# Performance work log

Measured on AMD Instinct MI355X. Metric: run time of the kernel, lower is better.

## Reference

```python
import jax, jax.numpy as jnp
import numpy as np

B, N, C = 16, 4096, 91            # images, proposals/image, classes (incl. background)
H, W = 800.0, 1333.0              # image shape
SCORE_THRESH = 0.05
NMS_THRESH = 0.5
K = 100                           # detections_per_img (greedy NMS steps)
M = 4096                          # top-M candidate prefilter before NMS
OFFSET = 1.0e4                    # class offset for batched NMS (>> max coord)
DW_CLAMP = float(np.log(1000.0 / 16.0))


def setup_inputs():
    key = jax.random.key(0)
    k1, k2, k3, k4, k5, k6 = jax.random.split(key, 6)
    class_logits = jax.random.normal(k1, (B * N, C), jnp.float32) * 2.0
    box_regression = jax.random.normal(k2, (B * N, C * 4), jnp.float32) * 0.1
    # valid proposal boxes (x1 < x2, y1 < y2, inside image)
    x1 = jax.random.uniform(k3, (B, N, 1)) * (W - 64.0)
    y1 = jax.random.uniform(k4, (B, N, 1)) * (H - 64.0)
    bw = jax.random.uniform(k5, (B, N, 1)) * 256.0 + 16.0
    bh = jax.random.uniform(k6, (B, N, 1)) * 256.0 + 16.0
    proposals = jnp.concatenate([x1, y1, jnp.minimum(x1 + bw, W), jnp.minimum(y1 + bh, H)], -1)
    return {"class_logits": class_logits, "box_regression": box_regression, "proposals": proposals}


def _decode_and_clip(rel, props):
    w = props[..., 2] - props[..., 0]
    h = props[..., 3] - props[..., 1]
    cx = props[..., 0] + 0.5 * w
    cy = props[..., 1] + 0.5 * h
    dx = rel[..., 0] / 10.0
    dy = rel[..., 1] / 10.0
    dw = jnp.minimum(rel[..., 2] / 5.0, DW_CLAMP)
    dh = jnp.minimum(rel[..., 3] / 5.0, DW_CLAMP)
    pcx = dx * w[..., None] + cx[..., None]
    pcy = dy * h[..., None] + cy[..., None]
    pw = jnp.exp(dw) * w[..., None]
    ph = jnp.exp(dh) * h[..., None]
    boxes = jnp.stack([
        jnp.clip(pcx - 0.5 * pw, 0.0, W),
        jnp.clip(pcy - 0.5 * ph, 0.0, H),
        jnp.clip(pcx + 0.5 * pw, 0.0, W),
        jnp.clip(pcy + 0.5 * ph, 0.0, H)], -1)  # [B,N,C,4]
    return boxes


def _greedy_nms(boxes, scores):
    # boxes: [M,4] (already class-offset), scores: [M] (suppressed entries == -1)
    x1, y1, x2, y2 = boxes[:, 0], boxes[:, 1], boxes[:, 2], boxes[:, 3]
    area = (x2 - x1) * (y2 - y1)

    def step(sc, _):
        i = jnp.argmax(sc)
        s = sc[i]
        valid = s > 0.0
        iw = jnp.clip(jnp.minimum(x2, x2[i]) - jnp.maximum(x1, x1[i]), 0.0)
        ih = jnp.clip(jnp.minimum(y2, y2[i]) - jnp.maximum(y1, y1[i]), 0.0)
        inter = iw * ih
        iou = inter / (area + area[i] - inter + 1e-9)
        sc = jnp.where((iou > NMS_THRESH) & valid, -1.0, sc)
        sc = sc.at[i].set(-1.0)
        return sc, (i, s, valid)

    _, (idx, ss, vv) = jax.lax.scan(step, scores, None, length=K)
    return idx, ss, vv


def _post_image(boxes_all, scores_all):
    # boxes_all: [N,C,4] decoded+clipped, scores_all: [N,C] softmax scores
    boxes = boxes_all[:, 1:, :].reshape(-1, 4)          # drop background class 0
    scores = scores_all[:, 1:].reshape(-1)              # [N*(C-1)], class fastest
    labels = jnp.tile(jnp.arange(1, C, dtype=jnp.int32), N)
    scores = jnp.where(scores > SCORE_THRESH, scores, -1.0)
    top_s, top_i = jax.lax.top_k(scores, M)
    b = boxes[top_i]
    l = labels[top_i]
    ob = b + (l.astype(jnp.float32) * OFFSET)[:, None]  # batched_nms class-offset trick
    idx, ss, vv = _greedy_nms(ob, top_s)
    out_boxes = jnp.where(vv[:, None], b[idx], 0.0)     # [K,4]
    out_scores = jnp.where(vv, ss, 0.0)                 # [K]
    out_labels = jnp.where(vv, l[idx], -1)              # [K]
    return out_boxes, out_scores, out_labels, vv


def reference(class_logits, box_regression, proposals):
    pred_scores = jax.nn.softmax(class_logits, -1).reshape(B, N, C)
    rel = box_regression.reshape(B, N, C, 4)
    pred_boxes = _decode_and_clip(rel, proposals)
    boxes, scores, labels, valid = jax.vmap(_post_image)(pred_boxes, pred_scores)
    return boxes, scores, labels, valid
```

## Files before the change

### kernel.cpp

```cpp
#include <hip/hip_runtime.h>

typedef unsigned long long u64;
typedef unsigned int u32;

#define BDIM 16
#define NP   4096
#define NC   91
#define NCM1 90
#define MSEL 4096
#define NSORT 1024
#define KOUT 100
#define RSLOT 19
#define CAP_D (NP * RSLOT)
#define SCORE_T 0.05f
#define NMS_T   0.5f
#define OFFSETF 10000.0f
#define DW_CLAMP_F 4.135166556742356f
#define WF 1333.0f
#define HF 800.0f
#define GTMIN 384
#define HCAP 4096
#define FKEY (((u64)0x3E800000u) << 32)

#define TN 1024
#define RPB 64

#define DECODE_BODY(kvar, bvar, BOXDST, PACKDST)                                   \
    {                                                                              \
        int flat = (int)(~(u32)(kvar));                                            \
        int nidx = flat / NCM1;                                                    \
        int c    = flat - nidx * NCM1 + 1;                                         \
        const float* pr = props + ((long)(bvar) * NP + nidx) * 4;                  \
        float x1 = pr[0], y1 = pr[1], x2 = pr[2], y2 = pr[3];                      \
        float w = x2 - x1, h = y2 - y1;                                            \
        float cx = x1 + 0.5f * w, cy = y1 + 0.5f * h;                              \
        const float* rr = boxreg + (((long)(bvar) * NP + nidx) * NC + c) * 4;      \
        float dx = rr[0] / 10.0f, dy = rr[1] / 10.0f;                              \
        float dw = fminf(rr[2] / 5.0f, DW_CLAMP_F);                                \
        float dh = fminf(rr[3] / 5.0f, DW_CLAMP_F);                                \
        float pcx = __fadd_rn(__fmul_rn(dx, w), cx);                               \
        float pcy = __fadd_rn(__fmul_rn(dy, h), cy);                               \
        float pw  = __fmul_rn(expf(dw), w);                                        \
        float ph2 = __fmul_rn(expf(dh), h);                                        \
        float bx1 = fminf(fmaxf(pcx - 0.5f * pw, 0.0f), WF);                       \
        float by1 = fminf(fmaxf(pcy - 0.5f * ph2, 0.0f), HF);                      \
        float bx2 = fminf(fmaxf(pcx + 0.5f * pw, 0.0f), WF);                       \
        float by2 = fminf(fmaxf(pcy + 0.5f * ph2, 0.0f), HF);                      \
        BOXDST = make_float4(bx1, by1, bx2, by2);                                  \
        float offB = (float)c * OFFSETF;                                           \
        float ox1 = bx1 + offB, oy1 = by1 + offB;                                  \
        float ox2 = bx2 + offB, oy2 = by2 + offB;                                  \
        PACKDST = make_float2((ox2 - ox1) * (oy2 - oy1), (float)c);                \
    }

__global__ __launch_bounds__(1024) void k_zero(int* __restrict__ gcount,
                                               int* __restrict__ hcnt,
                                               int* __restrict__ ghist) {
    int blk = blockIdx.x;
    if (blk == 0) {
        if (threadIdx.x < BDIM) gcount[threadIdx.x] = 0;
        if (threadIdx.x >= 64 && threadIdx.x < 64 + BDIM) hcnt[threadIdx.x - 64] = 0;
    } else {
        int* g = ghist + (blk - 1) * 2048;
        for (int i = threadIdx.x; i < 2048; i += 1024) g[i] = 0;
    }
}

__global__ __launch_bounds__(256) void k_soft(const float* __restrict__ logits,
                                              u64* __restrict__ dense,
                                              int* __restrict__ gcount,
                                              u64* __restrict__ hot,
                                              int* __restrict__ hcnt,
                                              int* __restrict__ ghist) {
    __shared__ u64 stage[RPB * RSLOT];
    __shared__ u64 hstage[256];
    __shared__ int lhist[2048];
    __shared__ int s_cnt, s_base, s_hcnt, s_hbase;

    int blk  = blockIdx.x;
    int b    = blk >> 6;
    int lane = threadIdx.x & 63;
    int wid  = threadIdx.x >> 6;

    if (threadIdx.x == 0) { s_cnt = 0; s_hcnt = 0; }
    for (int i = threadIdx.x; i < 2048; i += 256) lhist[i] = 0;
    __syncthreads();

    u64 lm = (1ull << lane) - 1ull;
    for (int it = 0; it < RPB / 4; ++it) {
        int row = blk * RPB + it * 4 + wid;
        const float* lg = logits + (long)row * NC;

        float v0 = lg[lane];
        float v1 = (lane < NC - 64) ? lg[64 + lane] : -3.0e38f;
        float mx = fmaxf(v0, v1);
#pragma unroll
        for (int s = 32; s; s >>= 1) mx = fmaxf(mx, __shfl_xor(mx, s));
        float e0 = expf(v0 - mx);
        float e1 = (lane < NC - 64) ? expf(v1 - mx) : 0.0f;
        float sum = e0 + e1;
#pragma unroll
        for (int s = 32; s; s >>= 1) sum += __shfl_xor(sum, s);

        float s0 = e0 / sum;
        float s1 = e1 / sum;

        int n = row & (NP - 1);
        bool p0 = (lane >= 1) && (s0 > SCORE_T);
        bool p1 = (lane < NC - 64) && (s1 > SCORE_T);
        u64 key0 = ((u64)__float_as_uint(s0) << 32) | (u32)(~(u32)(n * NCM1 + (lane - 1)));
        u64 key1 = ((u64)__float_as_uint(s1) << 32) | (u32)(~(u32)(n * NCM1 + (64 + lane - 1)));
        u64 m0 = __ballot(p0);
        u64 m1 = __ballot(p1);
        int c0  = __popcll(m0);
        int cnt = c0 + __popcll(m1);

        int base = 0;
        if (lane == 0 && cnt) base = atomicAdd(&s_cnt, cnt);
        base = __shfl(base, 0);
        if (p0) {
            stage[base + __popcll(m0 & lm)] = key0;
            atomicAdd(&lhist[(int)(key0 >> 53)], 1);
        }
        if (p1) {
            stage[base + c0 + __popcll(m1 & lm)] = key1;
            atomicAdd(&lhist[(int)(key1 >> 53)], 1);
        }

        bool q0 = p0 && (s0 >= 0.25f);
        bool q1 = p1 && (s1 >= 0.25f);
        u64 h0 = __ballot(q0);
        u64 h1 = __ballot(q1);
        int hc0 = __popcll(h0);
        int hrow = hc0 + __popcll(h1);
        int hb = 0;
        if (lane == 0 && hrow) hb = atomicAdd(&s_hcnt, hrow);
        hb = __shfl(hb, 0);
        if (q0) hstage[hb + __popcll(h0 & lm)] = key0;
        if (q1) hstage[hb + hc0 + __popcll(h1 & lm)] = key1;
    }
    __syncthreads();

    if (threadIdx.x == 0) {
        s_base  = atomicAdd(&gcount[b], s_cnt);
        s_hbase = atomicAdd(&hcnt[b], s_hcnt);
    }
    __syncthreads();
    int m = s_cnt, base = s_base;
    u64* kb = dense + (long)b * CAP_D + base;
    for (int i = threadIdx.x; i < m; i += 256) kb[i] = stage[i];
    int hm = s_hcnt, hb2 = s_hbase;
    u64* hbp = hot + (long)b * HCAP;
    for (int i = threadIdx.x; i < hm; i += 256) {
        int pos = hb2 + i;
        if (pos < HCAP) hbp[pos] = hstage[i];
    }
    for (int i = threadIdx.x; i < 2048; i += 256) {
        int v = lhist[i];
        if (v) atomicAdd(&ghist[b * 2048 + i], v);
    }
}

__device__ __forceinline__ u64 radix_rank(const u64* __restrict__ kb, int n, int rank,
                                          int* hist, int* p_sel, int* p_gt, int tid) {
    u64 prefix = 0, mask = 0;
    const int shifts[6] = {53, 42, 31, 20, 10, 0};
    const int bitsv [6] = {11, 11, 11, 11, 10, 10};

    for (int pass = 0; pass < 6; ++pass) {
        int shift = shifts[pass];
        int nb = 1 << bitsv[pass];
        if (tid < nb) hist[tid] = 0;
        if (tid + 1024 < nb) hist[tid + 1024] = 0;
        __syncthreads();
        for (int i = tid; i < n; i += 1024) {
            u64 k = kb[i];
            if ((k & mask) == prefix)
                atomicAdd(&hist[(int)((k >> shift) & (u64)(nb - 1))], 1);
        }
        __syncthreads();
        for (int d = 1; d < nb; d <<= 1) {
            int v0 = 0, v1 = 0;
            if (tid < nb && tid + d < nb) v0 = hist[tid + d];
            if (tid + 1024 < nb && tid + 1024 + d < nb) v1 = hist[tid + 1024 + d];
            __syncthreads();
            if (tid < nb) hist[tid] += v0;
            if (tid + 1024 < nb) hist[tid + 1024] += v1;
            __syncthreads();
        }
        for (int j = tid; j < nb; j += 1024) {
            int c  = hist[j];
            int cn = (j + 1 < nb) ? hist[j + 1] : 0;
            if (c >= rank && cn < rank) { *p_sel = j; *p_gt = cn; }
        }
        __syncthreads();
        prefix |= ((u64)(*p_sel)) << shift;
        mask   |= ((u64)(nb - 1)) << shift;
        rank   -= *p_gt;
        __syncthreads();
    }
    return prefix;
}

__device__ __forceinline__ u64 radix_upper(const u64* __restrict__ kb, int n, int rank,
                                           int* hist, int* p_sel, int* p_gt, int tid) {
    int rank0 = rank;
    u64 prefix = 0, mask = 0;
    const int shifts[6] = {53, 42, 31, 20, 10, 0};
    const int bitsv [6] = {11, 11, 11, 11, 10, 10};

    for (int pass = 0; pass < 6; ++pass) {
        int shift = shifts[pass];
        int nb = 1 << bitsv[pass];
        if (tid < nb) hist[tid] = 0;
        if (tid + 1024 < nb) hist[tid + 1024] = 0;
        __syncthreads();
        for (int i = tid; i < n; i += 1024) {
            u64 k = kb[i];
            if ((k & mask) == prefix)
                atomicAdd(&hist[(int)((k >> shift) & (u64)(nb - 1))], 1);
        }
        __syncthreads();
        for (int d = 1; d < nb; d <<= 1) {
            int v0 = 0, v1 = 0;
            if (tid < nb && tid + d < nb) v0 = hist[tid + d];
            if (tid + 1024 < nb && tid + 1024 + d < nb) v1 = hist[tid + 1024 + d];
            __syncthreads();
            if (tid < nb) hist[tid] += v0;
            if (tid + 1024 < nb) hist[tid + 1024] += v1;
            __syncthreads();
        }
        for (int j = tid; j < nb; j += 1024) {
            int c  = hist[j];
            int cn = (j + 1 < nb) ? hist[j + 1] : 0;
            if (c >= rank && cn < rank) { *p_sel = j; *p_gt = cn; }
        }
        __syncthreads();
        int sel = *p_sel, gt = *p_gt;
        rank -= gt;
        __syncthreads();
        if (pass < 5) {
            if (rank0 - rank >= GTMIN)
                return prefix + ((u64)(sel + 1) << shift);
            prefix |= ((u64)sel) << shift;
            mask   |= ((u64)(nb - 1)) << shift;
        } else {
            prefix |= ((u64)sel) << shift;
        }
    }
    return prefix;
}

__global__ __launch_bounds__(TN) void k_post(const u64* __restrict__ dense,
                                             const int* __restrict__ gcount,
                                             const u64* __restrict__ hot,
                                             const int* __restrict__ hcnt,
                                             const int* __restrict__ ghist,
                                             const float* __restrict__ boxreg,
                                             const float* __restrict__ props,
                                             float* __restrict__ out) {
    __shared__ __align__(16) char ldsbuf[131072];
    __shared__ int s_cnt, s_nacc, s_sel, s_gt;

    float4* sbox  = (float4*)ldsbuf;
    float2* spack = (float2*)(ldsbuf + 16384);
    u64*    skey  = (u64*)(ldsbuf + 24576);
    int*    hist  = (int*)(ldsbuf + 32768);

    int b = blockIdx.x, tid = threadIdx.x;
    int lane = tid & 63, wid = tid >> 6;
    int n = gcount[b]; if (n > CAP_D) n = CAP_D;
    const u64* kb = dense + (long)b * CAP_D;
    u64 lm = (1ull << lane) - 1ull;
    int npad = (n + TN - 1) & ~(TN - 1);

    u64 Bthr = 0ull;
    bool hist_ok = false;
    if (n > NSORT) {
        for (int i = tid; i < 2048; i += TN) hist[i] = ghist[b * 2048 + i];
        __syncthreads();
        for (int d = 1; d < 2048; d <<= 1) {
            int v0 = 0, v1 = 0;
            if (tid + d < 2048) v0 = hist[tid + d];
            if (tid + 1024 + d < 2048) v1 = hist[tid + 1024 + d];
            __syncthreads();
            hist[tid] += v0;
            if (tid + 1024 + d < 2048 || tid + 1024 < 2048) hist[tid + 1024] += v1;
            __syncthreads();
        }
        for (int j = tid; j < 2048; j += TN) {
            int c  = hist[j];
            int cn = (j + 1 < 2048) ? hist[j + 1] : 0;
            if (c >= NSORT && cn < NSORT) { s_sel = j; s_gt = cn; }
        }
        __syncthreads();
        int sel = s_sel, gt = s_gt;
        __syncthreads();
        if (gt >= GTMIN) { Bthr = ((u64)(sel + 1)) << 53; hist_ok = true; }
        else             Bthr = radix_upper(kb, n, NSORT, hist, &s_sel, &s_gt, tid);
    }
    int hn = hcnt[b];
    bool use_hot = hist_ok && (Bthr >= FKEY) && (hn <= HCAP);

    skey[tid] = 0ull;
    if (tid == 0) s_cnt = 0;
    __syncthreads();
    if (use_hot) {
        const u64* hb = hot + (long)b * HCAP;
        int hpad = (hn + TN - 1) & ~(TN - 1);
        for (int i0 = tid; i0 < hpad; i0 += TN) {
            bool inb = (i0 < hn);
            u64 k = inb ? hb[i0] : 0ull;
            bool pred = inb && (k >= Bthr);
            u64 mb_ = __ballot(pred);
            int cnt = __popcll(mb_);
            int bp = 0;
            if (lane == 0 && cnt) bp = atomicAdd(&s_cnt, cnt);
            bp = __shfl(bp, 0);
            if (pred) {
                int pos = bp + __popcll(mb_ & lm);
                if (pos < NSORT) skey[pos] = k;
            }
        }
    } else {
        for (int i0 = tid; i0 < npad; i0 += TN) {
            bool inb = (i0 < n);
            u64 k = inb ? kb[i0] : 0ull;
            bool pred = inb && (k >= Bthr);
            u64 mb_ = __ballot(pred);
            int cnt = __popcll(mb_);
            int bp = 0;
            if (lane == 0 && cnt) bp = atomicAdd(&s_cnt, cnt);
            bp = __shfl(bp, 0);
            if (pred) {
                int pos = bp + __popcll(mb_ & lm);
                if (pos < NSORT) skey[pos] = k;
            }
        }
    }
    __syncthreads();
    if (s_cnt > NSORT) {
        Bthr = radix_upper(kb, n, NSORT, hist, &s_sel, &s_gt, tid);
        skey[tid] = 0ull;
        if (tid == 0) s_cnt = 0;
        __syncthreads();
        for (int i0 = tid; i0 < npad; i0 += TN) {
            bool inb = (i0 < n);
            u64 k = inb ? kb[i0] : 0ull;
            bool pred = inb && (k >= Bthr);
            u64 mb_ = __ballot(pred);
            int cnt = __popcll(mb_);
            int bp = 0;
            if (lane == 0 && cnt) bp = atomicAdd(&s_cnt, cnt);
            bp = __shfl(bp, 0);
            if (pred) {
                int pos = bp + __popcll(mb_ & lm);
                if (pos < NSORT) skey[pos] = k;
            }
        }
        __syncthreads();
    }
    int mb = s_cnt; if (mb > NSORT) mb = NSORT;

    {
        u64 r = skey[tid];
        for (int kk = 2; kk <= NSORT; kk <<= 1) {
            for (int j = kk >> 1; j; j >>= 1) {
                u64 p;
                if (j >= 64) {
                    skey[tid] = r;
                    __syncthreads();
                    p = skey[tid ^ j];
                    __syncthreads();
                } else {
                    p = __shfl_xor(r, j);
                }
                bool lower = (tid & j) == 0;
                bool desc  = ((tid & kk) == 0);
                u64 mx = (r > p) ? r : p;
                u64 mn = (r > p) ? p : r;
                r = (lower == desc) ? mx : mn;
            }
        }
        skey[tid] = r;
        __syncthreads();
    }

    for (int i = tid; i < mb; i += TN) {
        u64 k = skey[i];
        float4 bx; float2 pk;
        DECODE_BODY(k, b, bx, pk);
        sbox[i] = bx;
        spack[i] = pk;
    }
    __syncthreads();

    float ax1_0 = 0, ay1_0 = 0, ax2_0 = 0, ay2_0 = 0, aar_0 = 0;
    float ax1_1 = 0, ay1_1 = 0, ax2_1 = 0, ay2_1 = 0, aar_1 = 0;
    int alb_0 = -1, alb_1 = -1;
    u64 aky_0 = 0, aky_1 = 0;
    int nacc = 0;

    if (wid == 0) {
        float4 Bv = sbox[0];
        float2 pk = spack[0];
        u64    ck = skey[0];
        for (int i = 0; i < mb && nacc < KOUT; ++i) {
            int ip = (i + 1 < mb) ? i + 1 : i;
            float4 nBv = sbox[ip];
            float2 npk = spack[ip];
            u64    nck = skey[ip];

            float areaB = pk.x;
            float labf  = pk.y;
            float off   = __fmul_rn(labf, OFFSETF);
            bool conf = false;
            if (lane < nacc && (float)alb_0 == labf) {
                float op1x = __fadd_rn(fminf(ax2_0, Bv.z), off);
                float op2x = __fadd_rn(fmaxf(ax1_0, Bv.x), off);
                float iw = fmaxf(op1x - op2x, 0.0f);
                float op1y = __fadd_rn(fminf(ay2_0, Bv.w), off);
                float op2y = __fadd_rn(fmaxf(ay1_0, Bv.y), off);
                float ih = fmaxf(op1y - op2y, 0.0f);
                float inter = iw * ih;
                float denom = areaB + aar_0 - inter + 1e-9f;
                if (inter / denom > NMS_T) conf = true;
            }
            if (64 + lane < nacc && (float)alb_1 == labf) {
                float op1x = __fadd_rn(fminf(ax2_1, Bv.z), off);
                float op2x = __fadd_rn(fmaxf(ax1_1, Bv.x), off);
                float iw = fmaxf(op1x - op2x, 0.0f);
                float op1y = __fadd_rn(fminf(ay2_1, Bv.w), off);
                float op2y = __fadd_rn(fmaxf(ay1_1, Bv.y), off);
                float ih = fmaxf(op1y - op2y, 0.0f);
                float inter = iw * ih;
                float denom = areaB + aar_1 - inter + 1e-9f;
                if (inter / denom > NMS_T) conf = true;
            }
            if (__ballot(conf) == 0ull) {
                if (nacc < 64) {
                    if (lane == nacc) {
                        ax1_0 = Bv.x; ay1_0 = Bv.y; ax2_0 = Bv.z; ay2_0 = Bv.w;
                        aar_0 = areaB; alb_0 = (int)labf; aky_0 = ck;
                    }
                } else {
                    if (lane == nacc - 64) {
                        ax1_1 = Bv.x; ay1_1 = Bv.y; ax2_1 = Bv.z; ay2_1 = Bv.w;
                        aar_1 = areaB; alb_1 = (int)labf; aky_1 = ck;
                    }
                }
                ++nacc;
            }
            Bv = nBv; pk = npk; ck = nck;
        }
        if (lane == 0) s_nacc = nacc;
    }
    __syncthreads();

    if (s_nacc < KOUT && Bthr != 0ull) {
        u64 T = 0ull;
        if (n > MSEL) T = radix_rank(kb, n, MSEL, hist, &s_sel, &s_gt, tid);

        u64*    fkey  = (u64*)ldsbuf;
        float4* fbox  = (float4*)(ldsbuf + 32768);
        float2* fpack = (float2*)(ldsbuf + 98304);

        for (int i = tid; i < MSEL; i += TN) fkey[i] = 0ull;
        if (tid == 0) s_cnt = 0;
        __syncthreads();
        for (int i0 = tid; i0 < npad; i0 += TN) {
            bool inb = (i0 < n);
            u64 k = inb ? kb[i0] : 0ull;
            bool pred = inb && (k >= T && k < Bthr);
            u64 mb_ = __ballot(pred);
            int cnt = __popcll(mb_);
            int bp = 0;
            if (lane == 0 && cnt) bp = atomicAdd(&s_cnt, cnt);
            bp = __shfl(bp, 0);
            if (pred) {
                int pos = bp + __popcll(mb_ & lm);
                if (pos < MSEL) fkey[pos] = k;
            }
        }
        __syncthreads();
        int mb2 = s_cnt; if (mb2 > MSEL) mb2 = MSEL;

        for (int kk = 2; kk <= MSEL; kk <<= 1) {
            for (int j = kk >> 1; j > 0; j >>= 1) {
                for (int t = tid; t < MSEL; t += TN) {
                    int l = t ^ j;
                    if (l > t) {
                        u64 a = fkey[t], c = fkey[l];
                        bool up = ((t & kk) == 0);
                        bool sw = up ? (a < c) : (a > c);
                        if (sw) { fkey[t] = c; fkey[l] = a; }
                    }
                }
                __syncthreads();
            }
        }

        for (int i = tid; i < mb2; i += TN) {
            u64 k = fkey[i];
            float4 bx; float2 pk;
            DECODE_BODY(k, b, bx, pk);
            fbox[i] = bx;
            fpack[i] = pk;
        }
        __syncthreads();

        if (wid == 0) {
            float4 Bv = fbox[0];
            float2 pk = fpack[0];
            u64    ck = fkey[0];
            for (int i = 0; i < mb2 && nacc < KOUT; ++i) {
                int ip = (i + 1 < mb2) ? i + 1 : i;
                float4 nBv = fbox[ip];
                float2 npk = fpack[ip];
                u64    nck = fkey[ip];

                float areaB = pk.x;
                float labf  = pk.y;
                float off   = __fmul_rn(labf, OFFSETF);
                bool conf = false;
                if (lane < nacc && (float)alb_0 == labf) {
                    float op1x = __fadd_rn(fminf(ax2_0, Bv.z), off);
                    float op2x = __fadd_rn(fmaxf(ax1_0, Bv.x), off);
                    float iw = fmaxf(op1x - op2x, 0.0f);
                    float op1y = __fadd_rn(fminf(ay2_0, Bv.w), off);
                    float op2y = __fadd_rn(fmaxf(ay1_0, Bv.y), off);
                    float ih = fmaxf(op1y - op2y, 0.0f);
                    float inter = iw * ih;
                    float denom = areaB + aar_0 - inter + 1e-9f;
                    if (inter / denom > NMS_T) conf = true;
                }
                if (64 + lane < nacc && (float)alb_1 == labf) {
                    float op1x = __fadd_rn(fminf(ax2_1, Bv.z), off);
                    float op2x = __fadd_rn(fmaxf(ax1_1, Bv.x), off);
                    float iw = fmaxf(op1x - op2x, 0.0f);
                    float op1y = __fadd_rn(fminf(ay2_1, Bv.w), off);
                    float op2y = __fadd_rn(fmaxf(ay1_1, Bv.y), off);
                    float ih = fmaxf(op1y - op2y, 0.0f);
                    float inter = iw * ih;
                    float denom = areaB + aar_1 - inter + 1e-9f;
                    if (inter / denom > NMS_T) conf = true;
                }
                if (__ballot(conf) == 0ull) {
                    if (nacc < 64) {
                        if (lane == nacc) {
                            ax1_0 = Bv.x; ay1_0 = Bv.y; ax2_0 = Bv.z; ay2_0 = Bv.w;
                            aar_0 = areaB; alb_0 = (int)labf; aky_0 = ck;
                        }
                    } else {
                        if (lane == nacc - 64) {
                            ax1_1 = Bv.x; ay1_1 = Bv.y; ax2_1 = Bv.z; ay2_1 = Bv.w;
                            aar_1 = areaB; alb_1 = (int)labf; aky_1 = ck;
                        }
                    }
                    ++nacc;
                }
                Bv = nBv; pk = npk; ck = nck;
            }
            if (lane == 0) s_nacc = nacc;
        }
        __syncthreads();
    }

    int na = s_nacc; if (na > KOUT) na = KOUT;
    if (wid == 0) {
        if (lane < na) {
            int a = lane;
            float* ob = out + ((long)b * KOUT + a) * 4;
            ob[0] = ax1_0; ob[1] = ay1_0; ob[2] = ax2_0; ob[3] = ay2_0;
            out[BDIM * KOUT * 4 + b * KOUT + a] = __uint_as_float((u32)(aky_0 >> 32));
            out[BDIM * KOUT * 5 + b * KOUT + a] = (float)alb_0;
            out[BDIM * KOUT * 6 + b * KOUT + a] = 1.0f;
        }
        if (64 + lane < na) {
            int a = 64 + lane;
            float* ob = out + ((long)b * KOUT + a) * 4;
            ob[0] = ax1_1; ob[1] = ay1_1; ob[2] = ax2_1; ob[3] = ay2_1;
            out[BDIM * KOUT * 4 + b * KOUT + a] = __uint_as_float((u32)(aky_1 >> 32));
            out[BDIM * KOUT * 5 + b * KOUT + a] = (float)alb_1;
            out[BDIM * KOUT * 6 + b * KOUT + a] = 1.0f;
        }
    }
    for (int a = tid; a < KOUT; a += TN) {
        if (a >= na) {
            float* ob = out + ((long)b * KOUT + a) * 4;
            ob[0] = 0.0f; ob[1] = 0.0f; ob[2] = 0.0f; ob[3] = 0.0f;
            out[BDIM * KOUT * 4 + b * KOUT + a] = 0.0f;
            out[BDIM * KOUT * 5 + b * KOUT + a] = -1.0f;
            out[BDIM * KOUT * 6 + b * KOUT + a] = 0.0f;
        }
    }
}

extern "C" void kernel_launch(void* const* d_in, const int* in_sizes, int n_in,
                              void* d_out, int out_size, void* d_ws, size_t ws_size,
                              hipStream_t stream) {
    const float* logits = (const float*)d_in[0];
    const float* boxreg = (const float*)d_in[1];
    const float* props  = (const float*)d_in[2];
    float* out = (float*)d_out;

    char* ws = (char*)d_ws;
    int* gcount = (int*)(ws + 0);
    int* hcnt   = (int*)(ws + 256);
    int* ghist  = (int*)(ws + 1024);
    u64* hot    = (u64*)(ws + 132096);
    u64* dense  = (u64*)(ws + 1048576);

    k_zero<<<17, 1024, 0, stream>>>(gcount, hcnt, ghist);
    k_soft<<<(BDIM * NP) / RPB, 256, 0, stream>>>(logits, dense, gcount, hot, hcnt, ghist);
    k_post<<<BDIM, TN, 0, stream>>>(dense, gcount, hot, hcnt, ghist, boxreg, props, out);
}
```

Measured before the change: 78.55 us.

## Precompute parallel IoU suppression bitmasks for first 128 candidates before greedy NMS

Each thread computes a 128-bit suppression mask against the first 128 sorted candidates in parallel. A single wavefront then runs greedy NMS with bitmask ANDs instead of per-step IoU and ballot. If all KOUT detections come from the first 128 candidates, the accepted boxes are gathered directly. Otherwise it falls back to the original serial loop. This adds an O(128·mb) parallel IoU pass and extra LDS use to shorten the serial dependency chain.

```diff
diff --git a/kernel.cpp b/kernel.cpp
--- a/kernel.cpp
+++ b/kernel.cpp
@@ -260,12 +260,15 @@
                                              const float* __restrict__ props,
                                              float* __restrict__ out) {
     __shared__ __align__(16) char ldsbuf[131072];
-    __shared__ int s_cnt, s_nacc, s_sel, s_gt;
+    __shared__ int s_cnt, s_nacc, s_sel, s_gt, s_ok;
+    __shared__ int s_ord[KOUT];
 
     float4* sbox  = (float4*)ldsbuf;
     float2* spack = (float2*)(ldsbuf + 16384);
     u64*    skey  = (u64*)(ldsbuf + 24576);
     int*    hist  = (int*)(ldsbuf + 32768);
+    u64*    mlo   = (u64*)(ldsbuf + 40960);
+    u64*    mhi   = (u64*)(ldsbuf + 49152);
 
     int b = blockIdx.x, tid = threadIdx.x;
     int lane = tid & 63, wid = tid >> 6;
@@ -395,129 +398,88 @@
     }
     __syncthreads();
 
+    {
+        int i = tid;
+        if (i < mb) {
+            float4 Bv = sbox[i];
+            float2 pk = spack[i];
+            float areaB = pk.x, labf = pk.y;
+            float off = __fmul_rn(labf, OFFSETF);
+            u64 lo = 0, hi = 0;
+            int jmax = (mb < 128) ? mb : 128;
+            for (int j = 0; j < jmax; ++j) {
+                if (j != i) {
+                    float2 tp = spack[j];
+                    if (tp.y == labf) {
+                        float4 Tv = sbox[j];
+                        float op1x = __fadd_rn(fminf(Tv.z, Bv.z), off);
+                        float op2x = __fadd_rn(fmaxf(Tv.x, Bv.x), off);
+                        float iw = fmaxf(op1x - op2x, 0.0f);
+                        float op1y = __fadd_rn(fminf(Tv.w, Bv.w), off);
+                        float op2y = __fadd_rn(fmaxf(Tv.y, Bv.y), off);
+                        float ih = fmaxf(op1y - op2y, 0.0f);
+                        float inter = iw * ih;
+                        float denom = areaB + tp.x - inter + 1e-9f;
+                        float iou = inter / denom;
+                        if (iou > NMS_T) { if (j < 64) lo |= 1ull << j; else hi |= 1ull << (j - 64); }
+                    }
+                }
+            }
+            mlo[i] = lo; mhi[i] = hi;
+        }
+    }
+    __syncthreads();
+
+    if (wid == 0) {
+        int fn = 0; int ok = 1;
+        u64 alo = 0, ahi = 0;
+        for (int i = 0; i < mb && fn < KOUT; ++i) {
+            u64 lo = mlo[i], hi = mhi[i];
+            if (((lo & alo) | (hi & ahi)) == 0ull) {
+                if (lane == 0) s_ord[fn] = i;
+                ++fn;
+                if (i < 64) alo |= 1ull << i;
+                else if (i < 128) ahi |= 1ull << (i - 64);
+                else if (fn < KOUT) { ok = 0; break; }
+            }
+        }
+        if (lane == 0) { s_nacc = fn; s_ok = ok; }
+    }
+    __syncthreads();
+
     float ax1_0 = 0, ay1_0 = 0, ax2_0 = 0, ay2_0 = 0, aar_0 = 0;
     float ax1_1 = 0, ay1_1 = 0, ax2_1 = 0, ay2_1 = 0, aar_1 = 0;
     int alb_0 = -1, alb_1 = -1;
     u64 aky_0 = 0, aky_1 = 0;
     int nacc = 0;
 
-    if (wid == 0) {
-        float4 Bv = sbox[0];
-        float2 pk = spack[0];
-        u64    ck = skey[0];
-        for (int i = 0; i < mb && nacc < KOUT; ++i) {
-            int ip = (i + 1 < mb) ? i + 1 : i;
-            float4 nBv = sbox[ip];
-            float2 npk = spack[ip];
-            u64    nck = skey[ip];
-
-            float areaB = pk.x;
-            float labf  = pk.y;
-            float off   = __fmul_rn(labf, OFFSETF);
-            bool conf = false;
-            if (lane < nacc && (float)alb_0 == labf) {
-                float op1x = __fadd_rn(fminf(ax2_0, Bv.z), off);
-                float op2x = __fadd_rn(fmaxf(ax1_0, Bv.x), off);
-                float iw = fmaxf(op1x - op2x, 0.0f);
-                float op1y = __fadd_rn(fminf(ay2_0, Bv.w), off);
-                float op2y = __fadd_rn(fmaxf(ay1_0, Bv.y), off);
-                float ih = fmaxf(op1y - op2y, 0.0f);
-                float inter = iw * ih;
-                float denom = areaB + aar_0 - inter + 1e-9f;
-                if (inter / denom > NMS_T) conf = true;
-            }
-            if (64 + lane < nacc && (float)alb_1 == labf) {
-                float op1x = __fadd_rn(fminf(ax2_1, Bv.z), off);
-                float op2x = __fadd_rn(fmaxf(ax1_1, Bv.x), off);
-                float iw = fmaxf(op1x - op2x, 0.0f);
-                float op1y = __fadd_rn(fminf(ay2_1, Bv.w), off);
-                float op2y = __fadd_rn(fmaxf(ay1_1, Bv.y), off);
-                float ih = fmaxf(op1y - op2y, 0.0f);
-                float inter = iw * ih;
-                float denom = areaB + aar_1 - inter + 1e-9f;
-                if (inter / denom > NMS_T) conf = true;
-            }
-            if (__ballot(conf) == 0ull) {
-                if (nacc < 64) {
-                    if (lane == nacc) {
-                        ax1_0 = Bv.x; ay1_0 = Bv.y; ax2_0 = Bv.z; ay2_0 = Bv.w;
-                        aar_0 = areaB; alb_0 = (int)labf; aky_0 = ck;
-                    }
-                } else {
-                    if (lane == nacc - 64) {
-                        ax1_1 = Bv.x; ay1_1 = Bv.y; ax2_1 = Bv.z; ay2_1 = Bv.w;
-                        aar_1 = areaB; alb_1 = (int)labf; aky_1 = ck;
-                    }
-                }
-                ++nacc;
-            }
-            Bv = nBv; pk = npk; ck = nck;
-        }
-        if (lane == 0) s_nacc = nacc;
-    }
-    __syncthreads();
-
-    if (s_nacc < KOUT && Bthr != 0ull) {
-        u64 T = 0ull;
-        if (n > MSEL) T = radix_rank(kb, n, MSEL, hist, &s_sel, &s_gt, tid);
-
-        u64*    fkey  = (u64*)ldsbuf;
-        float4* fbox  = (float4*)(ldsbuf + 32768);
-        float2* fpack = (float2*)(ldsbuf + 98304);
-
-        for (int i = tid; i < MSEL; i += TN) fkey[i] = 0ull;
-        if (tid == 0) s_cnt = 0;
-        __syncthreads();
-        for (int i0 = tid; i0 < npad; i0 += TN) {
-            bool inb = (i0 < n);
-            u64 k = inb ? kb[i0] : 0ull;
-            bool pred = inb && (k >= T && k < Bthr);
-            u64 mb_ = __ballot(pred);
-            int cnt = __popcll(mb_);
-            int bp = 0;
-            if (lane == 0 && cnt) bp = atomicAdd(&s_cnt, cnt);
-            bp = __shfl(bp, 0);
-            if (pred) {
-                int pos = bp + __popcll(mb_ & lm);
-                if (pos < MSEL) fkey[pos] = k;
-            }
-        }
-        __syncthreads();
-        int mb2 = s_cnt; if (mb2 > MSEL) mb2 = MSEL;
-
-        for (int kk = 2; kk <= MSEL; kk <<= 1) {
-            for (int j = kk >> 1; j > 0; j >>= 1) {
-                for (int t = tid; t < MSEL; t += TN) {
-                    int l = t ^ j;
-                    if (l > t) {
-                        u64 a = fkey[t], c = fkey[l];
-                        bool up = ((t & kk) == 0);
-                        bool sw = up ? (a < c) : (a > c);
-                        if (sw) { fkey[t] = c; fkey[l] = a; }
-                    }
-                }
-                __syncthreads();
-            }
-        }
-
-        for (int i = tid; i < mb2; i += TN) {
-            u64 k = fkey[i];
-            float4 bx; float2 pk;
-            DECODE_BODY(k, b, bx, pk);
-            fbox[i] = bx;
-            fpack[i] = pk;
-        }
-        __syncthreads();
-
+    if (s_ok) {
         if (wid == 0) {
-            float4 Bv = fbox[0];
-            float2 pk = fpack[0];
-            u64    ck = fkey[0];
-            for (int i = 0; i < mb2 && nacc < KOUT; ++i) {
-                int ip = (i + 1 < mb2) ? i + 1 : i;
-                float4 nBv = fbox[ip];
-                float2 npk = fpack[ip];
-                u64    nck = fkey[ip];
+            int fn = s_nacc;
+            if (lane < fn) {
+                int i = s_ord[lane];
+                float4 Bv = sbox[i]; float2 pk = spack[i];
+                ax1_0 = Bv.x; ay1_0 = Bv.y; ax2_0 = Bv.z; ay2_0 = Bv.w;
+                aar_0 = pk.x; alb_0 = (int)pk.y; aky_0 = skey[i];
+            }
+            if (64 + lane < fn) {
+                int i = s_ord[64 + lane];
+                float4 Bv = sbox[i]; float2 pk = spack[i];
+                ax1_1 = Bv.x; ay1_1 = Bv.y; ax2_1 = Bv.z; ay2_1 = Bv.w;
+                aar_1 = pk.x; alb_1 = (int)pk.y; aky_1 = skey[i];
+            }
+            nacc = fn;
+        }
+    } else {
+        if (wid == 0) {
+            float4 Bv = sbox[0];
+            float2 pk = spack[0];
+            u64    ck = skey[0];
+            for (int i = 0; i < mb && nacc < KOUT; ++i) {
+                int ip = (i + 1 < mb) ? i + 1 : i;
+                float4 nBv = sbox[ip];
+                float2 npk = spack[ip];
+                u64    nck = skey[ip];
 
                 float areaB = pk.x;
                 float labf  = pk.y;
@@ -563,6 +525,116 @@
             }
             if (lane == 0) s_nacc = nacc;
         }
+    }
+    __syncthreads();
+
+    if (s_nacc < KOUT && Bthr != 0ull) {
+        u64 T = 0ull;
+        if (n > MSEL) T = radix_rank(kb, n, MSEL, hist, &s_sel, &s_gt, tid);
+
+        u64*    fkey  = (u64*)ldsbuf;
+        float4* fbox  = (float4*)(ldsbuf + 32768);
+        float2* fpack = (float2*)(ldsbuf + 98304);
+
+        for (int i = tid; i < MSEL; i += TN) fkey[i] = 0ull;
+        if (tid == 0) s_cnt = 0;
+        __syncthreads();
+        for (int i0 = tid; i0 < npad; i0 += TN) {
+            bool inb = (i0 < n);
+            u64 k = inb ? kb[i0] : 0ull;
+            bool pred = inb && (k >= T && k < Bthr);
+            u64 mb_ = __ballot(pred);
+            int cnt = __popcll(mb_);
+            int bp = 0;
+            if (lane == 0 && cnt) bp = atomicAdd(&s_cnt, cnt);
+            bp = __shfl(bp, 0);
+            if (pred) {
+                int pos = bp + __popcll(mb_ & lm);
+                if (pos < MSEL) fkey[pos] = k;
+            }
+        }
+        __syncthreads();
+        int mb2 = s_cnt; if (mb2 > MSEL) mb2 = MSEL;
+
+        for (int kk = 2; kk <= MSEL; kk <<= 1) {
+            for (int j = kk >> 1; j > 0; j >>= 1) {
+                for (int t = tid; t < MSEL; t += TN) {
+                    int l = t ^ j;
+                    if (l > t) {
+                        u64 a = fkey[t], c = fkey[l];
+                        bool up = ((t & kk) == 0);
+                        bool sw = up ? (a < c) : (a > c);
+                        if (sw) { fkey[t] = c; fkey[l] = a; }
+                    }
+                }
+                __syncthreads();
+            }
+        }
+
+        for (int i = tid; i < mb2; i += TN) {
+            u64 k = fkey[i];
+            float4 bx; float2 pk;
+            DECODE_BODY(k, b, bx, pk);
+            fbox[i] = bx;
+            fpack[i] = pk;
+        }
+        __syncthreads();
+
+        if (wid == 0) {
+            nacc = s_nacc;
+            float4 Bv = fbox[0];
+            float2 pk = fpack[0];
+            u64    ck = fkey[0];
+            for (int i = 0; i < mb2 && nacc < KOUT; ++i) {
+                int ip = (i + 1 < mb2) ? i + 1 : i;
+                float4 nBv = fbox[ip];
+                float2 npk = fpack[ip];
+                u64    nck = fkey[ip];
+
+                float areaB = pk.x;
+                float labf  = pk.y;
+                float off   = __fmul_rn(labf, OFFSETF);
+                bool conf = false;
+                if (lane < nacc && (float)alb_0 == labf) {
+                    float op1x = __fadd_rn(fminf(ax2_0, Bv.z), off);
+                    float op2x = __fadd_rn(fmaxf(ax1_0, Bv.x), off);
+                    float iw = fmaxf(op1x - op2x, 0.0f);
+                    float op1y = __fadd_rn(fminf(ay2_0, Bv.w), off);
+                    float op2y = __fadd_rn(fmaxf(ay1_0, Bv.y), off);
+                    float ih = fmaxf(op1y - op2y, 0.0f);
+                    float inter = iw * ih;
+                    float denom = areaB + aar_0 - inter + 1e-9f;
+                    if (inter / denom > NMS_T) conf = true;
+                }
+                if (64 + lane < nacc && (float)alb_1 == labf) {
+                    float op1x = __fadd_rn(fminf(ax2_1, Bv.z), off);
+                    float op2x = __fadd_rn(fmaxf(ax1_1, Bv.x), off);
+                    float iw = fmaxf(op1x - op2x, 0.0f);
+                    float op1y = __fadd_rn(fminf(ay2_1, Bv.w), off);
+                    float op2y = __fadd_rn(fmaxf(ay1_1, Bv.y), off);
+                    float ih = fmaxf(op1y - op2y, 0.0f);
+                    float inter = iw * ih;
+                    float denom = areaB + aar_1 - inter + 1e-9f;
+                    if (inter / denom > NMS_T) conf = true;
+                }
+                if (__ballot(conf) == 0ull) {
+                    if (nacc < 64) {
+                        if (lane == nacc) {
+                            ax1_0 = Bv.x; ay1_0 = Bv.y; ax2_0 = Bv.z; ay2_0 = Bv.w;
+                            aar_0 = areaB; alb_0 = (int)labf; aky_0 = ck;
+                        }
+                    } else {
+                        if (lane == nacc - 64) {
+                            ax1_1 = Bv.x; ay1_1 = Bv.y; ax2_1 = Bv.z; ay2_1 = Bv.w;
+                            aar_1 = areaB; alb_1 = (int)labf; aky_1 = ck;
+                        }
+                    }
+                    ++nacc;
+                }
+                Bv = nBv; pk = npk; ck = nck;
+            }
+            if (lane == 0) s_nacc = nacc;
+        }
         __syncthreads();
     }
 
```

Measured after the change: 97.71 us. 1.24x slower.
